# Optimization experiments

Hardware: AMD Instinct MI355X
Metric: run time of the kernel (lower is better)

The kernel has to match this reference:

```python
import jax, jax.numpy as jnp
import numpy as np
from jax import lax

H = 1024
NH = 16
R = 32
B, S = 32, 1024
LN_EPS = 1e-5

def _gelu(x):
    return jax.nn.gelu(x, approximate=False)

def setup_inputs() -> dict:
    key = jax.random.key(0)
    ks = jax.random.split(key, 24)
    w = lambda k, shape: jax.random.normal(k, shape, jnp.float32) * 0.02
    d = {}
    d['computation_results'] = jax.random.normal(ks[0], (B, S, H), jnp.float32)
    d['max_steps'] = 16
    # rule selector: Linear(H,H), GELU, Linear(H,R)
    d['rule_w1'] = w(ks[1], (H, H)); d['rule_b1'] = jnp.zeros((H,))
    d['rule_w2'] = w(ks[2], (R, H)); d['rule_b2'] = jnp.zeros((R,))
    d['rule_emb'] = jax.random.normal(ks[3], (R, H), jnp.float32)
    # MultiheadAttention packed in-proj [3H,H] and out-proj [H,H]
    d['attn_in_w'] = w(ks[4], (3 * H, H)); d['attn_in_b'] = jnp.zeros((3 * H,))
    d['attn_out_w'] = w(ks[5], (H, H)); d['attn_out_b'] = jnp.zeros((H,))
    # 2-layer LSTM, PyTorch gate order i,f,g,o
    d['lstm_wih0'] = w(ks[6], (4 * H, H)); d['lstm_whh0'] = w(ks[7], (4 * H, H))
    d['lstm_bih0'] = jnp.zeros((4 * H,)); d['lstm_bhh0'] = jnp.zeros((4 * H,))
    d['lstm_wih1'] = w(ks[8], (4 * H, H)); d['lstm_whh1'] = w(ks[9], (4 * H, H))
    d['lstm_bih1'] = jnp.zeros((4 * H,)); d['lstm_bhh1'] = jnp.zeros((4 * H,))
    # step generator: Linear(H,2H), LayerNorm(2H), GELU, Linear(2H,H)
    d['gen_w1'] = w(ks[10], (2 * H, H)); d['gen_b1'] = jnp.zeros((2 * H,))
    d['gen_ln_g'] = jnp.ones((2 * H,)); d['gen_ln_b'] = jnp.zeros((2 * H,))
    d['gen_w2'] = w(ks[11], (H, 2 * H)); d['gen_b2'] = jnp.zeros((H,))
    # step validator: Linear(2H,H), GELU, Linear(H,1), Sigmoid
    d['val_w1'] = w(ks[12], (H, 2 * H)); d['val_b1'] = jnp.zeros((H,))
    d['val_w2'] = w(ks[13], (1, H)); d['val_b2'] = jnp.zeros((1,))
    # proof verifier: Linear(H,H), GELU, Linear(H,1), Sigmoid
    d['ver_w1'] = w(ks[14], (H, H)); d['ver_b1'] = jnp.zeros((H,))
    d['ver_w2'] = w(ks[15], (1, H)); d['ver_b2'] = jnp.zeros((1,))
    return d


def reference(computation_results, max_steps, rule_w1, rule_b1, rule_w2, rule_b2, rule_emb,
              attn_in_w, attn_in_b, attn_out_w, attn_out_b,
              lstm_wih0, lstm_whh0, lstm_bih0, lstm_bhh0,
              lstm_wih1, lstm_whh1, lstm_bih1, lstm_bhh1,
              gen_w1, gen_b1, gen_ln_g, gen_ln_b, gen_w2, gen_b2,
              val_w1, val_b1, val_w2, val_b2,
              ver_w1, ver_b1, ver_w2, ver_b2):
    comp = computation_results
    b, s, h = comp.shape
    dh = h // NH
    scale = dh ** -0.5
    wq, wk, wv = jnp.split(attn_in_w, 3, axis=0)
    bq, bk, bv = jnp.split(attn_in_b, 3, axis=0)
    # K/V projections of the static context, computed once outside the step loop
    K = (comp @ wk.T + bk).reshape(b, s, NH, dh)  # [B,S,NH,dh]
    V = (comp @ wv.T + bv).reshape(b, s, NH, dh)
    lstm_params = ((lstm_wih0, lstm_whh0, lstm_bih0, lstm_bhh0),
                   (lstm_wih1, lstm_whh1, lstm_bih1, lstm_bhh1))

    def step(carry, _):
        ps, hmem, cmem = carry  # ps: [B,H]; hmem/cmem: [2,B,H]
        # rule selection
        logits = _gelu(ps @ rule_w1.T + rule_b1) @ rule_w2.T + rule_b2
        probs = jax.nn.softmax(logits, axis=-1)  # [B,R]
        sel = probs @ rule_emb  # [B,H]
        # single-query multi-head attention over computation context
        q = (ps @ wq.T + bq).reshape(b, NH, dh) * scale
        scores = jnp.einsum('bhd,bshd->bhs', q, K)
        a = jax.nn.softmax(scores, axis=-1)  # [B,NH,S]
        ctx = jnp.einsum('bhs,bshd->bhd', a, V).reshape(b, h) @ attn_out_w.T + attn_out_b
        attn_avg = a.mean(axis=1)  # head-averaged weights, [B,S]
        # 2-layer LSTM cell, one timestep
        x = ps
        hs, cs = [], []
        for l, (wih, whh, bih, bhh) in enumerate(lstm_params):
            g = x @ wih.T + bih + hmem[l] @ whh.T + bhh
            gi, gf, gg, go = jnp.split(g, 4, axis=-1)
            cn = jax.nn.sigmoid(gf) * cmem[l] + jax.nn.sigmoid(gi) * jnp.tanh(gg)
            hn = jax.nn.sigmoid(go) * jnp.tanh(cn)
            hs.append(hn); cs.append(cn); x = hn
        mem_out = x
        # step generator with LayerNorm+GELU
        si = ps + sel + ctx + mem_out
        z = si @ gen_w1.T + gen_b1
        mu = z.mean(axis=-1, keepdims=True)
        var = ((z - mu) ** 2).mean(axis=-1, keepdims=True)
        z = (z - mu) / jnp.sqrt(var + LN_EPS) * gen_ln_g + gen_ln_b
        nxt = _gelu(z) @ gen_w2.T + gen_b2
        val = jax.nn.sigmoid(_gelu(jnp.concatenate([ps, nxt], axis=-1) @ val_w1.T + val_b1) @ val_w2.T + val_b2)
        return (nxt, jnp.stack(hs), jnp.stack(cs)), (nxt, probs, val, attn_avg)

    init_state = comp[:, 0, :]
    carry0 = (init_state, jnp.zeros((2, b, h), comp.dtype), jnp.zeros((2, b, h), comp.dtype))
    (final, _, _), (steps, probs, vals, attn) = lax.scan(step, carry0, None, length=int(max_steps))
    proof_steps = jnp.concatenate([init_state[None], steps], axis=0)  # [T+1,B,H]
    proof_validity = jax.nn.sigmoid(_gelu(final @ ver_w1.T + ver_b1) @ ver_w2.T + ver_b2)  # [B,1]
    return proof_steps, proof_validity, probs, vals, attn
```

## Files before the change

### kernel.cpp

```cpp
#include <hip/hip_runtime.h>

typedef unsigned short u16;
typedef unsigned int u32;
typedef __attribute__((ext_vector_type(8))) short short8v;
typedef __attribute__((ext_vector_type(4))) float f32x4;

#define MFMA16(a,b,c) __builtin_amdgcn_mfma_f32_16x16x32_bf16((a),(b),(c),0,0,0)

__device__ __forceinline__ u16 f2bf(float f){
  u32 u = __float_as_uint(f);
  return (u16)((u + 0x7fffu + ((u >> 16) & 1u)) >> 16);
}
__device__ __forceinline__ float bf2f(u16 h){ return __uint_as_float(((u32)h) << 16); }
__device__ __forceinline__ float gelu_f(float x){ return 0.5f * x * (1.f + erff(x * 0.70710678118654752f)); }
__device__ __forceinline__ float sigm_f(float x){ return 1.f / (1.f + __expf(-x)); }
__device__ __forceinline__ void acc4(float4& a, const float4 b){ a.x+=b.x; a.y+=b.y; a.z+=b.z; a.w+=b.w; }

__device__ __forceinline__ void gl16(const void* g, void* l){
  __builtin_amdgcn_global_load_lds((const __attribute__((address_space(1))) u32*)g,
                                   (__attribute__((address_space(3))) u32*)l, 16, 0, 0);
}

struct CastJobs { const float* s[12]; u16* d[12]; int start[13]; };
__global__ __launch_bounds__(256) void cast_all_k(CastJobs J){
  int bx = blockIdx.x, j = 0;
  #pragma unroll
  for (int t = 0; t < 12; t++) if (bx >= J.start[t + 1]) j = t + 1;
  int i = (bx - J.start[j]) * 1024 + threadIdx.x * 4;
  float4 v = *(const float4*)(J.s[j] + i);
  ushort4 o; o.x = f2bf(v.x); o.y = f2bf(v.y); o.z = f2bf(v.z); o.w = f2bf(v.w);
  *(ushort4*)(J.d[j] + i) = o;
}

__global__ __launch_bounds__(256) void cast_k(const float* __restrict__ s, u16* __restrict__ d, int n){
  int i = (blockIdx.x * 256 + threadIdx.x) * 4;
  if (i + 3 < n){
    float4 v = *(const float4*)(s + i);
    ushort4 o; o.x = f2bf(v.x); o.y = f2bf(v.y); o.z = f2bf(v.z); o.w = f2bf(v.w);
    *(ushort4*)(d + i) = o;
  }
}

__global__ __launch_bounds__(256) void tcast_k(const float* __restrict__ s, u16* __restrict__ d){
  __shared__ float tile[32][33];
  int bx = blockIdx.x & 31, by = blockIdx.x >> 5;
  int tx = threadIdx.x & 31, ty = threadIdx.x >> 5;
  #pragma unroll
  for (int i = 0; i < 4; i++)
    tile[ty + i * 8][tx] = s[(size_t)(by * 32 + ty + i * 8) * 1024 + bx * 32 + tx];
  __syncthreads();
  #pragma unroll
  for (int i = 0; i < 4; i++)
    d[(size_t)(bx * 32 + ty + i * 8) * 1024 + by * 32 + tx] = f2bf(tile[tx][ty + i * 8]);
}

__global__ __launch_bounds__(256) void bias2_k(const float* __restrict__ gw1, const float* __restrict__ aob,
                                               const float* __restrict__ gb1, float* __restrict__ out){
  int j = blockIdx.x * 32 + (threadIdx.x >> 3);
  int l8 = threadIdx.x & 7;
  const float* r = gw1 + (size_t)j * 1024;
  float acc = 0.f;
  #pragma unroll 8
  for (int kk = 0; kk < 32; kk++){
    int k = kk * 32 + l8 * 4;
    float4 a = *(const float4*)(r + k);
    float4 w = *(const float4*)(aob + k);
    acc += a.x * w.x + a.y * w.y + a.z * w.z + a.w * w.w;
  }
  acc += __shfl_xor(acc, 1); acc += __shfl_xor(acc, 2); acc += __shfl_xor(acc, 4);
  if (l8 == 0) out[j] = gb1[j] + acc;
}

__global__ __launch_bounds__(256) void init_k(const float* __restrict__ comp, float* ps0, float* outp,
                                              float* h0, float* c0, float* h1, float* c1){
  int i = blockIdx.x * 256 + threadIdx.x;
  int b = i >> 10, hh = i & 1023;
  float v = comp[(size_t)b * 1048576 + hh];
  ps0[i] = v; outp[i] = v;
  h0[i] = 0.f; c0[i] = 0.f; h1[i] = 0.f; c1[i] = 0.f;
}

__global__ __launch_bounds__(256) void gemmkv_k(const u16* __restrict__ compb,
    const u16* __restrict__ Wk, const u16* __restrict__ Wv,
    const float* __restrict__ bk, const float* __restrict__ bv,
    u16* __restrict__ Kt, u16* __restrict__ Vb)
{
  __shared__ u16 Sh[16384];
  u16* As = Sh;
  u16* Bs = Sh + 8192;
  int tid = threadIdx.x;
  int x = blockIdx.x;
  int xcd = x & 7, p = x >> 3;
  int cpanel = xcd * 32 + (p >> 3);
  int wpanel = p & 7;
  int isK = (blockIdx.z != 0);
  const u16 *msrc, *nsrc; int m0, n0;
  if (!isK){ m0 = cpanel * 128; n0 = wpanel * 128; msrc = compb; nsrc = Wv; }
  else     { m0 = wpanel * 128; n0 = cpanel * 128; msrc = Wk;    nsrc = compb; }

  int w = tid >> 6, l = tid & 63, lr = l & 15, lk = l >> 4;
  int wm = (w >> 1) * 64, wn = (w & 1) * 64;
  f32x4 acc[4][4];
  #pragma unroll
  for (int i = 0; i < 4; i++)
    #pragma unroll
    for (int j = 0; j < 4; j++) acc[i][j] = (f32x4){0.f,0.f,0.f,0.f};

  for (int kc = 0; kc < 1024; kc += 64){
    #pragma unroll
    for (int r = 0; r < 4; r++){
      int s = tid + r * 256;
      int row = s >> 3, pp = s & 7;
      int lg = pp ^ (row & 7);
      gl16(msrc + (size_t)(m0 + row) * 1024 + kc + lg * 8, As + s * 8);
      gl16(nsrc + (size_t)(n0 + row) * 1024 + kc + lg * 8, Bs + s * 8);
    }
    __syncthreads();
    #pragma unroll
    for (int kk = 0; kk < 2; kk++){
      short8v a[4], bb[4];
      #pragma unroll
      for (int mi = 0; mi < 4; mi++){
        int row = wm + mi * 16 + lr;
        int ph = (kk * 4 + lk) ^ (row & 7);
        a[mi] = *(const short8v*)(As + row * 64 + ph * 8);
      }
      #pragma unroll
      for (int ni = 0; ni < 4; ni++){
        int row = wn + ni * 16 + lr;
        int ph = (kk * 4 + lk) ^ (row & 7);
        bb[ni] = *(const short8v*)(Bs + row * 64 + ph * 8);
      }
      #pragma unroll
      for (int mi = 0; mi < 4; mi++)
        #pragma unroll
        for (int ni = 0; ni < 4; ni++)
          acc[mi][ni] = MFMA16(a[mi], bb[ni], acc[mi][ni]);
    }
    __syncthreads();
  }
  #pragma unroll
  for (int mi = 0; mi < 4; mi++)
    #pragma unroll
    for (int ni = 0; ni < 4; ni++)
      #pragma unroll
      for (int r = 0; r < 4; r++){
        int row = wm + mi * 16 + lk * 4 + r;
        int col = wn + ni * 16 + lr;
        float bias = isK ? bk[m0 + row] : bv[n0 + col];
        Sh[row * 128 + col] = f2bf(acc[mi][ni][r] + bias);
      }
  __syncthreads();
  u16* dst = isK ? Kt : Vb;
  size_t base = isK ? (((size_t)(n0 >> 10) * 1024 + m0) * 1024 + (n0 & 1023))
                    : ((size_t)m0 * 1024 + n0);
  for (int i = tid; i < 2048; i += 256){
    int r = i >> 4, c8 = (i & 15) * 8;
    *(uint4*)(dst + base + (size_t)r * 1024 + c8) = *(const uint4*)(Sh + r * 128 + c8);
  }
}

__global__ __launch_bounds__(256) void gemmbb_k(const u16* __restrict__ A, const u16* __restrict__ B,
                                                u16* __restrict__ C)
{
  __shared__ u16 As[128 * 64];
  __shared__ u16 Bs[128 * 64];
  int tid = threadIdx.x;
  int m0 = blockIdx.x * 128, n0 = blockIdx.y * 128;
  int w = tid >> 6, l = tid & 63, lr = l & 15, lk = l >> 4;
  int wm = (w >> 1) * 64, wn = (w & 1) * 64;
  f32x4 acc[4][4];
  #pragma unroll
  for (int i = 0; i < 4; i++)
    #pragma unroll
    for (int j = 0; j < 4; j++) acc[i][j] = (f32x4){0.f,0.f,0.f,0.f};
  for (int kc = 0; kc < 1024; kc += 64){
    #pragma unroll
    for (int r = 0; r < 4; r++){
      int s = tid + r * 256;
      int row = s >> 3, pp = s & 7;
      int lg = pp ^ (row & 7);
      gl16(A + (size_t)(m0 + row) * 1024 + kc + lg * 8, As + s * 8);
      gl16(B + (size_t)(n0 + row) * 1024 + kc + lg * 8, Bs + s * 8);
    }
    __syncthreads();
    #pragma unroll
    for (int kk = 0; kk < 2; kk++){
      short8v a[4], bb[4];
      #pragma unroll
      for (int mi = 0; mi < 4; mi++){
        int row = wm + mi * 16 + lr;
        int ph = (kk * 4 + lk) ^ (row & 7);
        a[mi] = *(const short8v*)(As + row * 64 + ph * 8);
      }
      #pragma unroll
      for (int ni = 0; ni < 4; ni++){
        int row = wn + ni * 16 + lr;
        int ph = (kk * 4 + lk) ^ (row & 7);
        bb[ni] = *(const short8v*)(Bs + row * 64 + ph * 8);
      }
      #pragma unroll
      for (int mi = 0; mi < 4; mi++)
        #pragma unroll
        for (int ni = 0; ni < 4; ni++)
          acc[mi][ni] = MFMA16(a[mi], bb[ni], acc[mi][ni]);
    }
    __syncthreads();
  }
  #pragma unroll
  for (int mi = 0; mi < 4; mi++)
    #pragma unroll
    for (int ni = 0; ni < 4; ni++)
      #pragma unroll
      for (int r = 0; r < 4; r++){
        int row = m0 + wm + mi * 16 + lk * 4 + r;
        int col = n0 + wn + ni * 16 + lr;
        C[(size_t)row * 1024 + col] = f2bf(acc[mi][ni][r]);
      }
}

struct LinSeg {
  const float* X0; const float* Xa; const float* Xb; const float* Xc;
  const u16* W1; const float* b1;
  const float* Y; const u16* W2; const float* b2;
  float* out; float* out2;
  int K1, ld1, K2, ld2, N, act, gate;
  float scale;
  float* stats;
  const float* lng; const float* lnb; const float* lnstats;
  const float* cprev; float* cout; float* hout;
};

__device__ __forceinline__ short8v pack8(float4 v0, float4 v1){
  short8v r;
  r[0]=(short)f2bf(v0.x); r[1]=(short)f2bf(v0.y); r[2]=(short)f2bf(v0.z); r[3]=(short)f2bf(v0.w);
  r[4]=(short)f2bf(v1.x); r[5]=(short)f2bf(v1.y); r[6]=(short)f2bf(v1.z); r[7]=(short)f2bf(v1.w);
  return r;
}

__device__ __forceinline__ short8v load_sum8(const LinSeg& S, int row, int kb){
  size_t o = (size_t)row * S.K1 + kb;
  float4 v0 = *(const float4*)(S.X0 + o);
  float4 v1 = *(const float4*)(S.X0 + o + 4);
  if (S.lng){
    float mu = S.lnstats[row] * (1.f / 2048.f);
    float ms = S.lnstats[32 + row] * (1.f / 2048.f);
    float rstd = rsqrtf(ms - mu * mu + 1e-5f);
    float4 g0 = *(const float4*)(S.lng + kb), g1 = *(const float4*)(S.lng + kb + 4);
    float4 b0 = *(const float4*)(S.lnb + kb), b1 = *(const float4*)(S.lnb + kb + 4);
    v0.x = gelu_f((v0.x - mu) * rstd * g0.x + b0.x);
    v0.y = gelu_f((v0.y - mu) * rstd * g0.y + b0.y);
    v0.z = gelu_f((v0.z - mu) * rstd * g0.z + b0.z);
    v0.w = gelu_f((v0.w - mu) * rstd * g0.w + b0.w);
    v1.x = gelu_f((v1.x - mu) * rstd * g1.x + b1.x);
    v1.y = gelu_f((v1.y - mu) * rstd * g1.y + b1.y);
    v1.z = gelu_f((v1.z - mu) * rstd * g1.z + b1.z);
    v1.w = gelu_f((v1.w - mu) * rstd * g1.w + b1.w);
  } else {
    if (S.Xa){ acc4(v0, *(const float4*)(S.Xa + o)); acc4(v1, *(const float4*)(S.Xa + o + 4)); }
    if (S.Xb){ acc4(v0, *(const float4*)(S.Xb + o)); acc4(v1, *(const float4*)(S.Xb + o + 4)); }
    if (S.Xc){ acc4(v0, *(const float4*)(S.Xc + o)); acc4(v1, *(const float4*)(S.Xc + o + 4)); }
  }
  return pack8(v0, v1);
}
__device__ __forceinline__ short8v load_y8(const float* p){
  return pack8(*(const float4*)(p), *(const float4*)(p + 4));
}

typedef float Red4[32][32];

__device__ void lin_body(const LinSeg& S, int bi, int tid, Red4* red){
  int c0 = bi * 32, j0 = bi * 8;
  int w = tid >> 6, l = tid & 63, lr = l & 15, lk = l >> 4;
  int wc0 = S.gate ? ((lr >> 3) << 10) + j0 + (lr & 7) : c0 + lr;
  int wc1 = S.gate ? (((lr + 16) >> 3) << 10) + j0 + ((lr + 16) & 7) : c0 + lr + 16;
  f32x4 acc[2][2];
  #pragma unroll
  for (int i = 0; i < 2; i++)
    #pragma unroll
    for (int j = 0; j < 2; j++) acc[i][j] = (f32x4){0.f,0.f,0.f,0.f};

  {
    int chunk = S.K1 >> 2;
    int kb0 = w * chunk + lk * 8;
    for (int kk = 0; kk < chunk; kk += 32){
      int kb = kb0 + kk;
      short8v a0 = load_sum8(S, lr, kb);
      short8v a1 = load_sum8(S, lr + 16, kb);
      short8v w0 = *(const short8v*)(S.W1 + (size_t)wc0 * S.ld1 + kb);
      short8v w1 = *(const short8v*)(S.W1 + (size_t)wc1 * S.ld1 + kb);
      acc[0][0] = MFMA16(a0, w0, acc[0][0]);
      acc[0][1] = MFMA16(a0, w1, acc[0][1]);
      acc[1][0] = MFMA16(a1, w0, acc[1][0]);
      acc[1][1] = MFMA16(a1, w1, acc[1][1]);
    }
  }
  if (S.Y){
    int chunk = S.K2 >> 2;
    int kb0 = w * chunk + lk * 8;
    for (int kk = 0; kk < chunk; kk += 32){
      int kb = kb0 + kk;
      short8v a0 = load_y8(S.Y + (size_t)lr * S.K2 + kb);
      short8v a1 = load_y8(S.Y + (size_t)(lr + 16) * S.K2 + kb);
      short8v w0 = *(const short8v*)(S.W2 + (size_t)wc0 * S.ld2 + kb);
      short8v w1 = *(const short8v*)(S.W2 + (size_t)wc1 * S.ld2 + kb);
      acc[0][0] = MFMA16(a0, w0, acc[0][0]);
      acc[0][1] = MFMA16(a0, w1, acc[0][1]);
      acc[1][0] = MFMA16(a1, w0, acc[1][0]);
      acc[1][1] = MFMA16(a1, w1, acc[1][1]);
    }
  }
  #pragma unroll
  for (int mi = 0; mi < 2; mi++)
    #pragma unroll
    for (int ni = 0; ni < 2; ni++)
      #pragma unroll
      for (int r = 0; r < 4; r++)
        red[w][mi * 16 + lk * 4 + r][ni * 16 + lr] = acc[mi][ni][r];
  __syncthreads();
  if (S.gate){
    int row = tid >> 3, j = tid & 7;
    float s[4];
    #pragma unroll
    for (int g = 0; g < 4; g++){
      float v = 0.f;
      #pragma unroll
      for (int ww = 0; ww < 4; ww++) v += red[ww][row][g * 8 + j];
      s[g] = v;
    }
    int gc = j0 + j;
    float gI = s[0] + S.b1[gc]        + S.b2[gc];
    float gF = s[1] + S.b1[1024 + gc] + S.b2[1024 + gc];
    float gG = s[2] + S.b1[2048 + gc] + S.b2[2048 + gc];
    float gO = s[3] + S.b1[3072 + gc] + S.b2[3072 + gc];
    int idx = row * 1024 + gc;
    float cN = sigm_f(gF) * S.cprev[idx] + sigm_f(gI) * tanhf(gG);
    S.cout[idx] = cN;
    S.hout[idx] = sigm_f(gO) * tanhf(cN);
    return;
  }
  float vout[4]; int iout[4];
  int cnt = 0;
  for (int i = tid; i < 1024; i += 256){
    int row = i >> 5, col = i & 31;
    float v = 0.f;
    #pragma unroll
    for (int ww = 0; ww < 4; ww++) v += red[ww][row][col];
    v += S.b1[c0 + col];
    if (S.b2) v += S.b2[c0 + col];
    if (S.act == 1) v = gelu_f(v);
    else if (S.act == 2) v *= S.scale;
    S.out[(size_t)row * S.N + c0 + col] = v;
    if (S.out2) S.out2[(size_t)row * S.N + c0 + col] = v;
    vout[cnt] = v; iout[cnt] = i; cnt++;
  }
  if (S.stats){
    __syncthreads();
    float* rf = (float*)red;
    #pragma unroll
    for (int q2 = 0; q2 < 4; q2++){
      rf[iout[q2]] = vout[q2];
      rf[1024 + iout[q2]] = vout[q2] * vout[q2];
    }
    __syncthreads();
    if (tid < 32){
      float s = 0.f, s2 = 0.f;
      #pragma unroll
      for (int cc = 0; cc < 32; cc++){ s += rf[tid * 32 + cc]; s2 += rf[1024 + tid * 32 + cc]; }
      atomicAdd(S.stats + tid, s);
      atomicAdd(S.stats + 32 + tid, s2);
    }
  }
}

__global__ __launch_bounds__(256) void linmulti_k(LinSeg s0, LinSeg s1, LinSeg s2, int n0, int n1){
  __shared__ float red[4][32][32];
  int bx = blockIdx.x, tid = threadIdx.x;
  if (bx < n0) lin_body(s0, bx, tid, red);
  else if (bx < n0 + n1) lin_body(s1, bx - n0, tid, red);
  else lin_body(s2, bx - n0 - n1, tid, red);
}

__device__ void attn_job(int bh, int tid, const float* q, const u16* Kt, const u16* Vb,
                         float* afull, float* ctx0, float* shf){
  float* qs = shf;
  float* sc = shf + 64;
  float* rmx = shf + 1088;
  float* rsm = shf + 1092;
  float* ctxp = shf + 1096;
  int b = bh >> 4, h = bh & 15;
  if (tid < 64) qs[tid] = q[bh * 64 + tid];
  __syncthreads();
  const u32* kt = (const u32*)(Kt + (size_t)bh * 65536);
  float a0 = 0.f, a1 = 0.f, a2 = 0.f, a3 = 0.f;
  #pragma unroll 8
  for (int d = 0; d < 64; d++){
    float qd = qs[d];
    u32 p0 = kt[d * 512 + tid];
    u32 p1 = kt[d * 512 + tid + 256];
    a0 += qd * bf2f((u16)(p0 & 0xffff)); a1 += qd * bf2f((u16)(p0 >> 16));
    a2 += qd * bf2f((u16)(p1 & 0xffff)); a3 += qd * bf2f((u16)(p1 >> 16));
  }
  float mx = fmaxf(fmaxf(a0, a1), fmaxf(a2, a3));
  for (int o = 1; o < 64; o <<= 1) mx = fmaxf(mx, __shfl_xor(mx, o));
  if ((tid & 63) == 0) rmx[tid >> 6] = mx;
  __syncthreads();
  mx = fmaxf(fmaxf(rmx[0], rmx[1]), fmaxf(rmx[2], rmx[3]));
  float e0 = __expf(a0 - mx), e1 = __expf(a1 - mx), e2 = __expf(a2 - mx), e3 = __expf(a3 - mx);
  float sm = e0 + e1 + e2 + e3;
  for (int o = 1; o < 64; o <<= 1) sm += __shfl_xor(sm, o);
  if ((tid & 63) == 0) rsm[tid >> 6] = sm;
  __syncthreads();
  sm = rsm[0] + rsm[1] + rsm[2] + rsm[3];
  float inv = 1.f / sm;
  float* ar = afull + (size_t)bh * 1024;
  float2 w0 = make_float2(e0 * inv, e1 * inv);
  float2 w1 = make_float2(e2 * inv, e3 * inv);
  *(float2*)(sc + 2 * tid) = w0;       *(float2*)(ar + 2 * tid) = w0;
  *(float2*)(sc + 512 + 2 * tid) = w1; *(float2*)(ar + 512 + 2 * tid) = w1;
  __syncthreads();
  int d2 = (tid & 31) * 2, chunk = tid >> 5;
  const u16* vb = Vb + ((size_t)(b * 1024) * 16 + h) * 64 + d2;
  float c0 = 0.f, c1 = 0.f;
  for (int s = chunk * 128; s < chunk * 128 + 128; s++){
    u32 vv = *(const u32*)(vb + (size_t)s * 1024);
    float wv = sc[s];
    c0 += wv * bf2f((u16)(vv & 0xffff));
    c1 += wv * bf2f((u16)(vv >> 16));
  }
  *(float2*)(ctxp + chunk * 64 + d2) = make_float2(c0, c1);
  __syncthreads();
  if (tid < 64){
    float r = 0.f;
    #pragma unroll
    for (int c = 0; c < 8; c++) r += ctxp[c * 64 + tid];
    ctx0[bh * 64 + tid] = r;
  }
}

__device__ void rule2_job(int b, int tid, const float* h1a, const float* w2, const float* b2,
                          const float* emb, float* probs_out, float* sel, float* shf){
  float* lg = shf;
  float* psh = shf + 32;
  int j = tid >> 3, l8 = tid & 7;
  const float* xr = h1a + b * 1024;
  const float* wr = w2 + j * 1024;
  float acc = 0.f;
  #pragma unroll 8
  for (int kk = 0; kk < 32; kk++){
    int k = kk * 32 + l8 * 4;
    float4 xv = *(const float4*)(xr + k);
    float4 wv = *(const float4*)(wr + k);
    acc += xv.x * wv.x + xv.y * wv.y + xv.z * wv.z + xv.w * wv.w;
  }
  acc += __shfl_xor(acc, 1); acc += __shfl_xor(acc, 2); acc += __shfl_xor(acc, 4);
  if (l8 == 0) lg[j] = acc + b2[j];
  __syncthreads();
  if (tid < 32){
    float v = lg[tid];
    float m = v;
    for (int o = 1; o < 32; o <<= 1) m = fmaxf(m, __shfl_xor(m, o));
    float e = __expf(v - m);
    float s = e;
    for (int o = 1; o < 32; o <<= 1) s += __shfl_xor(s, o);
    float p = e / s;
    psh[tid] = p;
    probs_out[b * 32 + tid] = p;
  }
  __syncthreads();
  for (int j2 = tid; j2 < 1024; j2 += 256){
    float a2 = 0.f;
    #pragma unroll
    for (int r = 0; r < 32; r++) a2 += psh[r] * emb[r * 1024 + j2];
    sel[b * 1024 + j2] = a2;
  }
}

struct D2Params {
  const float* qbuf;
  const u16* Kt; const u16* Vb; float* afull; float* ctx0;
  const float* h1a; const float* w2; const float* b2r; const float* emb;
  float* probs_out; float* sel;
  LinSeg sL1; float* lnstats;
};
__global__ __launch_bounds__(256) void step_d2_k(D2Params P){
  __shared__ float red[4][32][32];
  float* shf = &red[0][0][0];
  int bx = blockIdx.x, tid = threadIdx.x;
  if (bx < 512){ attn_job(bx, tid, P.qbuf, P.Kt, P.Vb, P.afull, P.ctx0, shf); return; }
  if (bx < 544){ rule2_job(bx - 512, tid, P.h1a, P.w2, P.b2r, P.emb, P.probs_out, P.sel, shf); return; }
  if (bx < 672){ lin_body(P.sL1, bx - 544, tid, red); return; }
  if (tid < 64) P.lnstats[tid] = 0.f;
}

__global__ __launch_bounds__(256) void valver_k(const u16* __restrict__ vw1, const float* __restrict__ vb1,
    const u16* __restrict__ verw1, const float* __restrict__ verb1,
    const float* __restrict__ proof, float* __restrict__ v1){
  __shared__ float red[4][32][32];
  int t = blockIdx.y;
  LinSeg S = {};
  if (t < 16){
    S.X0 = proof + (size_t)t * 32768; S.K1 = 1024; S.W1 = vw1; S.ld1 = 2048; S.b1 = vb1;
    S.Y = proof + (size_t)(t + 1) * 32768; S.K2 = 1024; S.W2 = vw1 + 1024; S.ld2 = 2048;
  } else {
    S.X0 = proof + (size_t)16 * 32768; S.K1 = 1024; S.W1 = verw1; S.ld1 = 1024; S.b1 = verb1;
  }
  S.out = v1 + (size_t)t * 32768; S.N = 1024; S.act = 1;
  lin_body(S, blockIdx.x, threadIdx.x, red);
}

__global__ __launch_bounds__(256) void dotsig_b_k(const float* __restrict__ v1,
    const float* __restrict__ w2v, const float* __restrict__ b2v,
    const float* __restrict__ w2ver, const float* __restrict__ b2ver,
    float* __restrict__ out_vals, float* __restrict__ out_valid){
  int t = blockIdx.x;
  const float* w = (t < 16) ? w2v : w2ver;
  const float* bs = (t < 16) ? b2v : b2ver;
  const float* x = v1 + (size_t)t * 32768;
  int b = threadIdx.x >> 3, l8 = threadIdx.x & 7;
  const float* xr = x + (size_t)b * 1024;
  float acc = 0.f;
  #pragma unroll 8
  for (int kk = 0; kk < 32; kk++){
    int k = kk * 32 + l8 * 4;
    float4 xv = *(const float4*)(xr + k);
    float4 wv = *(const float4*)(w + k);
    acc += xv.x * wv.x + xv.y * wv.y + xv.z * wv.z + xv.w * wv.w;
  }
  acc += __shfl_xor(acc, 1); acc += __shfl_xor(acc, 2); acc += __shfl_xor(acc, 4);
  if (l8 == 0){
    float r = sigm_f(acc + bs[0]);
    if (t < 16) out_vals[t * 32 + b] = r; else out_valid[b] = r;
  }
}

__global__ __launch_bounds__(256) void attnavg_all_k(const float* __restrict__ afull, float* __restrict__ out){
  int idx = blockIdx.x * 256 + threadIdx.x;
  int t = idx >> 15, r = idx & 32767;
  int b = r >> 10, s = r & 1023;
  const float* base = afull + (size_t)t * 524288 + (size_t)b * 16384;
  float acc = 0.f;
  #pragma unroll
  for (int h = 0; h < 16; h++) acc += base[h * 1024 + s];
  out[idx] = acc * (1.f / 16.f);
}

extern "C" void kernel_launch(void* const* d_in, const int* in_sizes, int n_in,
                              void* d_out, int out_size, void* d_ws, size_t ws_size,
                              hipStream_t stream) {
  const float* comp      = (const float*)d_in[0];
  const float* rule_w1   = (const float*)d_in[2];
  const float* rule_b1   = (const float*)d_in[3];
  const float* rule_w2   = (const float*)d_in[4];
  const float* rule_b2   = (const float*)d_in[5];
  const float* rule_emb  = (const float*)d_in[6];
  const float* attn_in_w = (const float*)d_in[7];
  const float* attn_in_b = (const float*)d_in[8];
  const float* attn_out_w= (const float*)d_in[9];
  const float* attn_out_b= (const float*)d_in[10];
  const float* wih0 = (const float*)d_in[11];
  const float* whh0 = (const float*)d_in[12];
  const float* bih0 = (const float*)d_in[13];
  const float* bhh0 = (const float*)d_in[14];
  const float* wih1 = (const float*)d_in[15];
  const float* whh1 = (const float*)d_in[16];
  const float* bih1 = (const float*)d_in[17];
  const float* bhh1 = (const float*)d_in[18];
  const float* gen_w1 = (const float*)d_in[19];
  const float* gen_b1 = (const float*)d_in[20];
  const float* ln_g   = (const float*)d_in[21];
  const float* ln_b   = (const float*)d_in[22];
  const float* gen_w2 = (const float*)d_in[23];
  const float* gen_b2 = (const float*)d_in[24];
  const float* val_w1 = (const float*)d_in[25];
  const float* val_b1 = (const float*)d_in[26];
  const float* val_w2 = (const float*)d_in[27];
  const float* val_b2 = (const float*)d_in[28];
  const float* ver_w1 = (const float*)d_in[29];
  const float* ver_b1 = (const float*)d_in[30];
  const float* ver_w2 = (const float*)d_in[31];
  const float* ver_b2 = (const float*)d_in[32];

  float* out_f     = (float*)d_out;
  float* out_proof = out_f;
  float* out_valid = out_f + 17 * 32768;
  float* out_probs = out_valid + 32;
  float* out_vals  = out_probs + 16 * 1024;
  float* out_attn  = out_vals + 16 * 32;

  char* wp = (char*)d_ws;
  auto carve = [&](size_t bytes) -> void* {
    void* p = (void*)wp; wp += (bytes + 255) & ~(size_t)255; return p;
  };
  u16* Kt    = (u16*)carve((size_t)33554432 * 2);
  u16* Vb    = (u16*)carve((size_t)33554432 * 2);
  u16* compb = (u16*)carve((size_t)33554432 * 2);
  float* afull_all = (float*)compb;
  u16* rw1b  = (u16*)carve(2097152);
  u16* wqb   = (u16*)carve(2097152);
  u16* wkb   = (u16*)carve(2097152);
  u16* wvb   = (u16*)carve(2097152);
  u16* aowTb = (u16*)carve(2097152);
  u16* wih0b = (u16*)carve(8388608);
  u16* whh0b = (u16*)carve(8388608);
  u16* wih1b = (u16*)carve(8388608);
  u16* whh1b = (u16*)carve(8388608);
  u16* gw1b  = (u16*)carve(4194304);
  u16* gw2b  = (u16*)carve(4194304);
  u16* vw1b  = (u16*)carve(4194304);
  u16* verw1b= (u16*)carve(2097152);
  u16* gaw   = (u16*)carve(4194304);
  float* bias2 = (float*)carve(8192);
  float* psb[2]  = { (float*)carve(131072), (float*)carve(131072) };
  float* h0b[2]  = { (float*)carve(131072), (float*)carve(131072) };
  float* c0b[2]  = { (float*)carve(131072), (float*)carve(131072) };
  float* h1b[2]  = { (float*)carve(131072), (float*)carve(131072) };
  float* c1b[2]  = { (float*)carve(131072), (float*)carve(131072) };
  float* h1act = (float*)carve(131072);
  float* sel   = (float*)carve(131072);
  float* qbuf  = (float*)carve(131072);
  float* ctx0  = (float*)carve(131072);
  float* zbuf  = (float*)carve(262144);
  float* v1buf = (float*)carve(2228224);
  float* lnstats = (float*)carve(256);
  (void)ws_size; (void)in_sizes; (void)n_in; (void)out_size;

  CastJobs J;
  const float* srcs[12] = { rule_w1, attn_in_w, attn_in_w + 1048576, attn_in_w + 2097152,
                            wih0, whh0, wih1, whh1, gen_w1, gen_w2, val_w1, ver_w1 };
  u16* dsts[12] = { rw1b, wqb, wkb, wvb, wih0b, whh0b, wih1b, whh1b, gw1b, gw2b, vw1b, verw1b };
  int sizes[12] = { 1048576, 1048576, 1048576, 1048576,
                    4194304, 4194304, 4194304, 4194304, 2097152, 2097152, 2097152, 1048576 };
  int st = 0;
  for (int i = 0; i < 12; i++){ J.s[i] = srcs[i]; J.d[i] = dsts[i]; J.start[i] = st; st += sizes[i] / 1024; }
  J.start[12] = st;
  cast_all_k<<<dim3(st), dim3(256), 0, stream>>>(J);
  tcast_k<<<dim3(1024), dim3(256), 0, stream>>>(attn_out_w, aowTb);
  cast_k<<<dim3(32768), dim3(256), 0, stream>>>(comp, compb, 33554432);

  gemmkv_k<<<dim3(2048, 1, 2), dim3(256), 0, stream>>>(compb, wkb, wvb,
      attn_in_b + 1024, attn_in_b + 2048, Kt, Vb);
  gemmbb_k<<<dim3(16, 8), dim3(256), 0, stream>>>(gw1b, aowTb, gaw);
  bias2_k<<<dim3(64), dim3(256), 0, stream>>>(gen_w1, attn_out_b, gen_b1, bias2);

  init_k<<<dim3(128), dim3(256), 0, stream>>>(comp, psb[0], out_proof,
      h0b[0], c0b[0], h1b[0], c1b[0]);

  for (int t = 0; t < 16; t++){
    int cur = t & 1, nx = cur ^ 1;
    float* ps = psb[cur];
    float* afull_t = afull_all + (size_t)t * 524288;
    LinSeg sRule = {}; sRule.X0 = ps; sRule.K1 = 1024; sRule.W1 = rw1b; sRule.ld1 = 1024;
    sRule.b1 = rule_b1; sRule.out = h1act; sRule.N = 1024; sRule.act = 1;
    LinSeg sQ = {}; sQ.X0 = ps; sQ.K1 = 1024; sQ.W1 = wqb; sQ.ld1 = 1024; sQ.b1 = attn_in_b;
    sQ.out = qbuf; sQ.N = 1024; sQ.act = 2; sQ.scale = 0.125f;
    LinSeg sL0 = {}; sL0.X0 = ps; sL0.K1 = 1024; sL0.W1 = wih0b; sL0.ld1 = 1024; sL0.b1 = bih0;
    sL0.Y = h0b[cur]; sL0.K2 = 1024; sL0.W2 = whh0b; sL0.ld2 = 1024; sL0.b2 = bhh0;
    sL0.gate = 1; sL0.cprev = c0b[cur]; sL0.cout = c0b[nx]; sL0.hout = h0b[nx];
    linmulti_k<<<dim3(192), dim3(256), 0, stream>>>(sRule, sQ, sL0, 32, 32);
    D2Params P;
    P.qbuf = qbuf;
    P.Kt = Kt; P.Vb = Vb; P.afull = afull_t; P.ctx0 = ctx0;
    P.h1a = h1act; P.w2 = rule_w2; P.b2r = rule_b2; P.emb = rule_emb;
    P.probs_out = out_probs + t * 1024; P.sel = sel;
    LinSeg sL1 = {}; sL1.X0 = h0b[nx]; sL1.K1 = 1024; sL1.W1 = wih1b; sL1.ld1 = 1024; sL1.b1 = bih1;
    sL1.Y = h1b[cur]; sL1.K2 = 1024; sL1.W2 = whh1b; sL1.ld2 = 1024; sL1.b2 = bhh1;
    sL1.gate = 1; sL1.cprev = c1b[cur]; sL1.cout = c1b[nx]; sL1.hout = h1b[nx];
    P.sL1 = sL1; P.lnstats = lnstats;
    step_d2_k<<<dim3(673), dim3(256), 0, stream>>>(P);
    LinSeg sG1 = {}; sG1.X0 = ps; sG1.Xa = sel; sG1.Xb = h1b[nx];
    sG1.K1 = 1024; sG1.W1 = gw1b; sG1.ld1 = 1024; sG1.b1 = bias2;
    sG1.Y = ctx0; sG1.K2 = 1024; sG1.W2 = gaw; sG1.ld2 = 1024;
    sG1.out = zbuf; sG1.N = 2048; sG1.stats = lnstats;
    linmulti_k<<<dim3(64), dim3(256), 0, stream>>>(sG1, sG1, sG1, 64, 0);
    LinSeg sG2 = {}; sG2.X0 = zbuf; sG2.K1 = 2048; sG2.W1 = gw2b; sG2.ld1 = 2048; sG2.b1 = gen_b2;
    sG2.out = psb[nx]; sG2.N = 1024; sG2.out2 = out_proof + (size_t)(t + 1) * 32768;
    sG2.lng = ln_g; sG2.lnb = ln_b; sG2.lnstats = lnstats;
    linmulti_k<<<dim3(32), dim3(256), 0, stream>>>(sG2, sG2, sG2, 32, 0);
  }
  valver_k<<<dim3(32, 17), dim3(256), 0, stream>>>(vw1b, val_b1, verw1b, ver_b1, out_proof, v1buf);
  dotsig_b_k<<<dim3(17), dim3(256), 0, stream>>>(v1buf, val_w2, val_b2, ver_w2, ver_b2,
      out_vals, out_valid);
  attnavg_all_k<<<dim3(2048), dim3(256), 0, stream>>>(afull_all, out_attn);
}
```

Baseline: 2.105 ms.

## Halve per-block tile width, split gen2 along K, and relayout V per head

```diff
diff --git a/kernel.cpp b/kernel.cpp
--- a/kernel.cpp
+++ b/kernel.cpp
@@ -21,24 +21,15 @@
                                    (__attribute__((address_space(3))) u32*)l, 16, 0, 0);
 }
 
-struct CastJobs { const float* s[12]; u16* d[12]; int start[13]; };
+struct CastJobs { const float* s[13]; u16* d[13]; int start[14]; };
 __global__ __launch_bounds__(256) void cast_all_k(CastJobs J){
   int bx = blockIdx.x, j = 0;
   #pragma unroll
-  for (int t = 0; t < 12; t++) if (bx >= J.start[t + 1]) j = t + 1;
+  for (int t = 0; t < 13; t++) if (bx >= J.start[t + 1]) j = t + 1;
   int i = (bx - J.start[j]) * 1024 + threadIdx.x * 4;
   float4 v = *(const float4*)(J.s[j] + i);
   ushort4 o; o.x = f2bf(v.x); o.y = f2bf(v.y); o.z = f2bf(v.z); o.w = f2bf(v.w);
   *(ushort4*)(J.d[j] + i) = o;
-}
-
-__global__ __launch_bounds__(256) void cast_k(const float* __restrict__ s, u16* __restrict__ d, int n){
-  int i = (blockIdx.x * 256 + threadIdx.x) * 4;
-  if (i + 3 < n){
-    float4 v = *(const float4*)(s + i);
-    ushort4 o; o.x = f2bf(v.x); o.y = f2bf(v.y); o.z = f2bf(v.z); o.w = f2bf(v.w);
-    *(ushort4*)(d + i) = o;
-  }
 }
 
 __global__ __launch_bounds__(256) void tcast_k(const float* __restrict__ s, u16* __restrict__ d){
@@ -71,12 +62,12 @@
   if (l8 == 0) out[j] = gb1[j] + acc;
 }
 
-__global__ __launch_bounds__(256) void init_k(const float* __restrict__ comp, float* ps0, float* outp,
-                                              float* h0, float* c0, float* h1, float* c1){
+__global__ __launch_bounds__(256) void init_k(const float* __restrict__ comp, float* psa, float* psbz,
+                                              float* outp, float* h0, float* c0, float* h1, float* c1){
   int i = blockIdx.x * 256 + threadIdx.x;
   int b = i >> 10, hh = i & 1023;
   float v = comp[(size_t)b * 1048576 + hh];
-  ps0[i] = v; outp[i] = v;
+  psa[i] = v; psbz[i] = 0.f; outp[i] = v;
   h0[i] = 0.f; c0[i] = 0.f; h1[i] = 0.f; c1[i] = 0.f;
 }
 
@@ -151,12 +142,19 @@
         Sh[row * 128 + col] = f2bf(acc[mi][ni][r] + bias);
       }
   __syncthreads();
-  u16* dst = isK ? Kt : Vb;
-  size_t base = isK ? (((size_t)(n0 >> 10) * 1024 + m0) * 1024 + (n0 & 1023))
-                    : ((size_t)m0 * 1024 + n0);
   for (int i = tid; i < 2048; i += 256){
     int r = i >> 4, c8 = (i & 15) * 8;
-    *(uint4*)(dst + base + (size_t)r * 1024 + c8) = *(const uint4*)(Sh + r * 128 + c8);
+    uint4 o = *(const uint4*)(Sh + r * 128 + c8);
+    if (!isK){
+      int bs = m0 + r, hd = n0 + c8;
+      int b = bs >> 10, s = bs & 1023;
+      int h = hd >> 6, d = hd & 63;
+      *(uint4*)(Vb + ((size_t)(b * 16 + h) * 1024 + s) * 64 + d) = o;
+    } else {
+      int hd = m0 + r, bs = n0 + c8;
+      int b = bs >> 10, s = bs & 1023;
+      *(uint4*)(Kt + ((size_t)b * 1024 + hd) * 1024 + s) = o;
+    }
   }
 }
 
@@ -224,7 +222,7 @@
   const u16* W1; const float* b1;
   const float* Y; const u16* W2; const float* b2;
   float* out; float* out2;
-  int K1, ld1, K2, ld2, N, act, gate;
+  int K1, ldx, ld1, K2, ld2, N, act, gate;
   float scale;
   float* stats;
   const float* lng; const float* lnb; const float* lnstats;
@@ -239,7 +237,7 @@
 }
 
 __device__ __forceinline__ short8v load_sum8(const LinSeg& S, int row, int kb){
-  size_t o = (size_t)row * S.K1 + kb;
+  size_t o = (size_t)row * S.ldx + kb;
   float4 v0 = *(const float4*)(S.X0 + o);
   float4 v1 = *(const float4*)(S.X0 + o + 4);
   if (S.lng){
@@ -267,18 +265,15 @@
   return pack8(*(const float4*)(p), *(const float4*)(p + 4));
 }
 
-typedef float Red4[32][32];
-
-__device__ void lin_body(const LinSeg& S, int bi, int tid, Red4* red){
-  int c0 = bi * 32, j0 = bi * 8;
+typedef float Red16[32][16];
+
+__device__ void lin_body(const LinSeg& S, int bi, int tid, Red16* red){
+  int c0 = bi * 16, j0 = bi * 4;
   int w = tid >> 6, l = tid & 63, lr = l & 15, lk = l >> 4;
-  int wc0 = S.gate ? ((lr >> 3) << 10) + j0 + (lr & 7) : c0 + lr;
-  int wc1 = S.gate ? (((lr + 16) >> 3) << 10) + j0 + ((lr + 16) & 7) : c0 + lr + 16;
-  f32x4 acc[2][2];
-  #pragma unroll
-  for (int i = 0; i < 2; i++)
-    #pragma unroll
-    for (int j = 0; j < 2; j++) acc[i][j] = (f32x4){0.f,0.f,0.f,0.f};
+  int wc0 = S.gate ? ((lr >> 2) << 10) + j0 + (lr & 3) : c0 + lr;
+  f32x4 acc[2];
+  acc[0] = (f32x4){0.f,0.f,0.f,0.f};
+  acc[1] = (f32x4){0.f,0.f,0.f,0.f};
 
   {
     int chunk = S.K1 >> 2;
@@ -288,11 +283,8 @@
       short8v a0 = load_sum8(S, lr, kb);
       short8v a1 = load_sum8(S, lr + 16, kb);
       short8v w0 = *(const short8v*)(S.W1 + (size_t)wc0 * S.ld1 + kb);
-      short8v w1 = *(const short8v*)(S.W1 + (size_t)wc1 * S.ld1 + kb);
-      acc[0][0] = MFMA16(a0, w0, acc[0][0]);
-      acc[0][1] = MFMA16(a0, w1, acc[0][1]);
-      acc[1][0] = MFMA16(a1, w0, acc[1][0]);
-      acc[1][1] = MFMA16(a1, w1, acc[1][1]);
+      acc[0] = MFMA16(a0, w0, acc[0]);
+      acc[1] = MFMA16(a1, w0, acc[1]);
     }
   }
   if (S.Y){
@@ -303,50 +295,47 @@
       short8v a0 = load_y8(S.Y + (size_t)lr * S.K2 + kb);
       short8v a1 = load_y8(S.Y + (size_t)(lr + 16) * S.K2 + kb);
       short8v w0 = *(const short8v*)(S.W2 + (size_t)wc0 * S.ld2 + kb);
-      short8v w1 = *(const short8v*)(S.W2 + (size_t)wc1 * S.ld2 + kb);
-      acc[0][0] = MFMA16(a0, w0, acc[0][0]);
-      acc[0][1] = MFMA16(a0, w1, acc[0][1]);
-      acc[1][0] = MFMA16(a1, w0, acc[1][0]);
-      acc[1][1] = MFMA16(a1, w1, acc[1][1]);
+      acc[0] = MFMA16(a0, w0, acc[0]);
+      acc[1] = MFMA16(a1, w0, acc[1]);
     }
   }
   #pragma unroll
   for (int mi = 0; mi < 2; mi++)
     #pragma unroll
-    for (int ni = 0; ni < 2; ni++)
-      #pragma unroll
-      for (int r = 0; r < 4; r++)
-        red[w][mi * 16 + lk * 4 + r][ni * 16 + lr] = acc[mi][ni][r];
+    for (int r = 0; r < 4; r++)
+      red[w][mi * 16 + lk * 4 + r][lr] = acc[mi][r];
   __syncthreads();
   if (S.gate){
-    int row = tid >> 3, j = tid & 7;
-    float s[4];
-    #pragma unroll
-    for (int g = 0; g < 4; g++){
-      float v = 0.f;
-      #pragma unroll
-      for (int ww = 0; ww < 4; ww++) v += red[ww][row][g * 8 + j];
-      s[g] = v;
-    }
-    int gc = j0 + j;
-    float gI = s[0] + S.b1[gc]        + S.b2[gc];
-    float gF = s[1] + S.b1[1024 + gc] + S.b2[1024 + gc];
-    float gG = s[2] + S.b1[2048 + gc] + S.b2[2048 + gc];
-    float gO = s[3] + S.b1[3072 + gc] + S.b2[3072 + gc];
-    int idx = row * 1024 + gc;
-    float cN = sigm_f(gF) * S.cprev[idx] + sigm_f(gI) * tanhf(gG);
-    S.cout[idx] = cN;
-    S.hout[idx] = sigm_f(gO) * tanhf(cN);
+    if (tid < 128){
+      int row = tid >> 2, j = tid & 3;
+      float s[4];
+      #pragma unroll
+      for (int g = 0; g < 4; g++){
+        float v = 0.f;
+        #pragma unroll
+        for (int ww = 0; ww < 4; ww++) v += red[ww][row][g * 4 + j];
+        s[g] = v;
+      }
+      int gc = j0 + j;
+      float gI = s[0] + S.b1[gc]        + S.b2[gc];
+      float gF = s[1] + S.b1[1024 + gc] + S.b2[1024 + gc];
+      float gG = s[2] + S.b1[2048 + gc] + S.b2[2048 + gc];
+      float gO = s[3] + S.b1[3072 + gc] + S.b2[3072 + gc];
+      int idx = row * 1024 + gc;
+      float cN = sigm_f(gF) * S.cprev[idx] + sigm_f(gI) * tanhf(gG);
+      S.cout[idx] = cN;
+      S.hout[idx] = sigm_f(gO) * tanhf(cN);
+    }
     return;
   }
-  float vout[4]; int iout[4];
+  float vout[2]; int iout[2];
   int cnt = 0;
-  for (int i = tid; i < 1024; i += 256){
-    int row = i >> 5, col = i & 31;
+  for (int i = tid; i < 512; i += 256){
+    int row = i >> 4, col = i & 15;
     float v = 0.f;
     #pragma unroll
     for (int ww = 0; ww < 4; ww++) v += red[ww][row][col];
-    v += S.b1[c0 + col];
+    if (S.b1) v += S.b1[c0 + col];
     if (S.b2) v += S.b2[c0 + col];
     if (S.act == 1) v = gelu_f(v);
     else if (S.act == 2) v *= S.scale;
@@ -357,16 +346,13 @@
   if (S.stats){
     __syncthreads();
     float* rf = (float*)red;
-    #pragma unroll
-    for (int q2 = 0; q2 < 4; q2++){
-      rf[iout[q2]] = vout[q2];
-      rf[1024 + iout[q2]] = vout[q2] * vout[q2];
-    }
+    rf[iout[0]] = vout[0]; rf[512 + iout[0]] = vout[0] * vout[0];
+    rf[iout[1]] = vout[1]; rf[512 + iout[1]] = vout[1] * vout[1];
     __syncthreads();
     if (tid < 32){
       float s = 0.f, s2 = 0.f;
       #pragma unroll
-      for (int cc = 0; cc < 32; cc++){ s += rf[tid * 32 + cc]; s2 += rf[1024 + tid * 32 + cc]; }
+      for (int cc = 0; cc < 16; cc++){ s += rf[tid * 16 + cc]; s2 += rf[512 + tid * 16 + cc]; }
       atomicAdd(S.stats + tid, s);
       atomicAdd(S.stats + 32 + tid, s2);
     }
@@ -374,7 +360,7 @@
 }
 
 __global__ __launch_bounds__(256) void linmulti_k(LinSeg s0, LinSeg s1, LinSeg s2, int n0, int n1){
-  __shared__ float red[4][32][32];
+  __shared__ float red[4][32][16];
   int bx = blockIdx.x, tid = threadIdx.x;
   if (bx < n0) lin_body(s0, bx, tid, red);
   else if (bx < n0 + n1) lin_body(s1, bx - n0, tid, red);
@@ -385,8 +371,7 @@
                          float* afull, float* ctx0, float* shf){
   float* qs = shf;
   float* sc = shf + 64;
-  float* rmx = shf + 1088;
-  float* rsm = shf + 1092;
+  float* rr = shf + 1088;
   float* ctxp = shf + 1096;
   int b = bh >> 4, h = bh & 15;
   if (tid < 64) qs[tid] = q[bh * 64 + tid];
@@ -403,15 +388,15 @@
   }
   float mx = fmaxf(fmaxf(a0, a1), fmaxf(a2, a3));
   for (int o = 1; o < 64; o <<= 1) mx = fmaxf(mx, __shfl_xor(mx, o));
-  if ((tid & 63) == 0) rmx[tid >> 6] = mx;
-  __syncthreads();
-  mx = fmaxf(fmaxf(rmx[0], rmx[1]), fmaxf(rmx[2], rmx[3]));
+  if ((tid & 63) == 0) rr[tid >> 6] = mx;
+  __syncthreads();
+  mx = fmaxf(fmaxf(rr[0], rr[1]), fmaxf(rr[2], rr[3]));
   float e0 = __expf(a0 - mx), e1 = __expf(a1 - mx), e2 = __expf(a2 - mx), e3 = __expf(a3 - mx);
   float sm = e0 + e1 + e2 + e3;
   for (int o = 1; o < 64; o <<= 1) sm += __shfl_xor(sm, o);
-  if ((tid & 63) == 0) rsm[tid >> 6] = sm;
-  __syncthreads();
-  sm = rsm[0] + rsm[1] + rsm[2] + rsm[3];
+  if ((tid & 63) == 0) rr[4 + (tid >> 6)] = sm;
+  __syncthreads();
+  sm = rr[4] + rr[5] + rr[6] + rr[7];
   float inv = 1.f / sm;
   float* ar = afull + (size_t)bh * 1024;
   float2 w0 = make_float2(e0 * inv, e1 * inv);
@@ -419,16 +404,18 @@
   *(float2*)(sc + 2 * tid) = w0;       *(float2*)(ar + 2 * tid) = w0;
   *(float2*)(sc + 512 + 2 * tid) = w1; *(float2*)(ar + 512 + 2 * tid) = w1;
   __syncthreads();
-  int d2 = (tid & 31) * 2, chunk = tid >> 5;
-  const u16* vb = Vb + ((size_t)(b * 1024) * 16 + h) * 64 + d2;
+  int dd2 = tid & 31, chunk = tid >> 5;
+  const u32* vp = (const u32*)(Vb + ((size_t)(b * 16 + h) * 1024 + chunk * 128) * 64) + dd2;
+  const float* scp = sc + chunk * 128;
   float c0 = 0.f, c1 = 0.f;
-  for (int s = chunk * 128; s < chunk * 128 + 128; s++){
-    u32 vv = *(const u32*)(vb + (size_t)s * 1024);
-    float wv = sc[s];
-    c0 += wv * bf2f((u16)(vv & 0xffff));
-    c1 += wv * bf2f((u16)(vv >> 16));
-  }
-  *(float2*)(ctxp + chunk * 64 + d2) = make_float2(c0, c1);
+  #pragma unroll 8
+  for (int s = 0; s < 128; s++){
+    u32 vv = vp[s * 32];
+    float w = scp[s];
+    c0 += w * bf2f((u16)(vv & 0xffff));
+    c1 += w * bf2f((u16)(vv >> 16));
+  }
+  *(float2*)(ctxp + chunk * 64 + dd2 * 2) = make_float2(c0, c1);
   __syncthreads();
   if (tid < 64){
     float r = 0.f;
@@ -476,6 +463,20 @@
   }
 }
 
+__global__ __launch_bounds__(256) void step_d1_k(LinSeg sRule, LinSeg sQ, LinSeg sL0,
+                                                 const float* pa, const float* pb, float* proof_t){
+  __shared__ float red[4][32][16];
+  int bx = blockIdx.x, tid = threadIdx.x;
+  if (bx < 64){ lin_body(sRule, bx, tid, red); return; }
+  if (bx < 128){ lin_body(sQ, bx - 64, tid, red); return; }
+  if (bx < 384){ lin_body(sL0, bx - 128, tid, red); return; }
+  int i = (bx - 384) * 1024 + tid * 4;
+  float4 va = *(const float4*)(pa + i);
+  float4 vb = *(const float4*)(pb + i);
+  acc4(va, vb);
+  *(float4*)(proof_t + i) = va;
+}
+
 struct D2Params {
   const float* qbuf;
   const u16* Kt; const u16* Vb; float* afull; float* ctx0;
@@ -484,26 +485,36 @@
   LinSeg sL1; float* lnstats;
 };
 __global__ __launch_bounds__(256) void step_d2_k(D2Params P){
-  __shared__ float red[4][32][32];
+  __shared__ float red[4][32][16];
   float* shf = &red[0][0][0];
   int bx = blockIdx.x, tid = threadIdx.x;
   if (bx < 512){ attn_job(bx, tid, P.qbuf, P.Kt, P.Vb, P.afull, P.ctx0, shf); return; }
   if (bx < 544){ rule2_job(bx - 512, tid, P.h1a, P.w2, P.b2r, P.emb, P.probs_out, P.sel, shf); return; }
-  if (bx < 672){ lin_body(P.sL1, bx - 544, tid, red); return; }
+  if (bx < 800){ lin_body(P.sL1, bx - 544, tid, red); return; }
   if (tid < 64) P.lnstats[tid] = 0.f;
+}
+
+__global__ __launch_bounds__(256) void fixup_k(const float* __restrict__ pa, const float* __restrict__ pb,
+                                               float* __restrict__ out){
+  int i = blockIdx.x * 1024 + threadIdx.x * 4;
+  float4 va = *(const float4*)(pa + i);
+  float4 vb = *(const float4*)(pb + i);
+  acc4(va, vb);
+  *(float4*)(out + i) = va;
 }
 
 __global__ __launch_bounds__(256) void valver_k(const u16* __restrict__ vw1, const float* __restrict__ vb1,
     const u16* __restrict__ verw1, const float* __restrict__ verb1,
-    const float* __restrict__ proof, float* __restrict__ v1){
-  __shared__ float red[4][32][32];
+    const float* __restrict__ proof, const float* __restrict__ pfa, const float* __restrict__ pfb,
+    float* __restrict__ v1){
+  __shared__ float red[4][32][16];
   int t = blockIdx.y;
   LinSeg S = {};
   if (t < 16){
-    S.X0 = proof + (size_t)t * 32768; S.K1 = 1024; S.W1 = vw1; S.ld1 = 2048; S.b1 = vb1;
+    S.X0 = proof + (size_t)t * 32768; S.K1 = 1024; S.ldx = 1024; S.W1 = vw1; S.ld1 = 2048; S.b1 = vb1;
     S.Y = proof + (size_t)(t + 1) * 32768; S.K2 = 1024; S.W2 = vw1 + 1024; S.ld2 = 2048;
   } else {
-    S.X0 = proof + (size_t)16 * 32768; S.K1 = 1024; S.W1 = verw1; S.ld1 = 1024; S.b1 = verb1;
+    S.X0 = pfa; S.Xa = pfb; S.K1 = 1024; S.ldx = 1024; S.W1 = verw1; S.ld1 = 1024; S.b1 = verb1;
   }
   S.out = v1 + (size_t)t * 32768; S.N = 1024; S.act = 1;
   lin_body(S, blockIdx.x, threadIdx.x, red);
@@ -611,11 +622,12 @@
   u16* verw1b= (u16*)carve(2097152);
   u16* gaw   = (u16*)carve(4194304);
   float* bias2 = (float*)carve(8192);
-  float* psb[2]  = { (float*)carve(131072), (float*)carve(131072) };
-  float* h0b[2]  = { (float*)carve(131072), (float*)carve(131072) };
-  float* c0b[2]  = { (float*)carve(131072), (float*)carve(131072) };
-  float* h1b[2]  = { (float*)carve(131072), (float*)carve(131072) };
-  float* c1b[2]  = { (float*)carve(131072), (float*)carve(131072) };
+  float* psa[2] = { (float*)carve(131072), (float*)carve(131072) };
+  float* psq[2] = { (float*)carve(131072), (float*)carve(131072) };
+  float* h0b[2] = { (float*)carve(131072), (float*)carve(131072) };
+  float* c0b[2] = { (float*)carve(131072), (float*)carve(131072) };
+  float* h1b[2] = { (float*)carve(131072), (float*)carve(131072) };
+  float* c1b[2] = { (float*)carve(131072), (float*)carve(131072) };
   float* h1act = (float*)carve(131072);
   float* sel   = (float*)carve(131072);
   float* qbuf  = (float*)carve(131072);
@@ -626,59 +638,68 @@
   (void)ws_size; (void)in_sizes; (void)n_in; (void)out_size;
 
   CastJobs J;
-  const float* srcs[12] = { rule_w1, attn_in_w, attn_in_w + 1048576, attn_in_w + 2097152,
-                            wih0, whh0, wih1, whh1, gen_w1, gen_w2, val_w1, ver_w1 };
-  u16* dsts[12] = { rw1b, wqb, wkb, wvb, wih0b, whh0b, wih1b, whh1b, gw1b, gw2b, vw1b, verw1b };
-  int sizes[12] = { 1048576, 1048576, 1048576, 1048576,
-                    4194304, 4194304, 4194304, 4194304, 2097152, 2097152, 2097152, 1048576 };
+  const float* srcs[13] = { rule_w1, attn_in_w, attn_in_w + 1048576, attn_in_w + 2097152,
+                            wih0, whh0, wih1, whh1, gen_w1, gen_w2, val_w1, ver_w1, comp };
+  u16* dsts[13] = { rw1b, wqb, wkb, wvb, wih0b, whh0b, wih1b, whh1b, gw1b, gw2b, vw1b, verw1b, compb };
+  int sizes[13] = { 1048576, 1048576, 1048576, 1048576,
+                    4194304, 4194304, 4194304, 4194304, 2097152, 2097152, 2097152, 1048576, 33554432 };
   int st = 0;
-  for (int i = 0; i < 12; i++){ J.s[i] = srcs[i]; J.d[i] = dsts[i]; J.start[i] = st; st += sizes[i] / 1024; }
-  J.start[12] = st;
+  for (int i = 0; i < 13; i++){ J.s[i] = srcs[i]; J.d[i] = dsts[i]; J.start[i] = st; st += sizes[i] / 1024; }
+  J.start[13] = st;
   cast_all_k<<<dim3(st), dim3(256), 0, stream>>>(J);
   tcast_k<<<dim3(1024), dim3(256), 0, stream>>>(attn_out_w, aowTb);
-  cast_k<<<dim3(32768), dim3(256), 0, stream>>>(comp, compb, 33554432);
 
   gemmkv_k<<<dim3(2048, 1, 2), dim3(256), 0, stream>>>(compb, wkb, wvb,
       attn_in_b + 1024, attn_in_b + 2048, Kt, Vb);
   gemmbb_k<<<dim3(16, 8), dim3(256), 0, stream>>>(gw1b, aowTb, gaw);
   bias2_k<<<dim3(64), dim3(256), 0, stream>>>(gen_w1, attn_out_b, gen_b1, bias2);
 
-  init_k<<<dim3(128), dim3(256), 0, stream>>>(comp, psb[0], out_proof,
+  init_k<<<dim3(128), dim3(256), 0, stream>>>(comp, psa[0], psq[0], out_proof,
       h0b[0], c0b[0], h1b[0], c1b[0]);
 
   for (int t = 0; t < 16; t++){
     int cur = t & 1, nx = cur ^ 1;
-    float* ps = psb[cur];
+    float* pa = psa[cur];
+    float* pb = psq[cur];
     float* afull_t = afull_all + (size_t)t * 524288;
-    LinSeg sRule = {}; sRule.X0 = ps; sRule.K1 = 1024; sRule.W1 = rw1b; sRule.ld1 = 1024;
-    sRule.b1 = rule_b1; sRule.out = h1act; sRule.N = 1024; sRule.act = 1;
-    LinSeg sQ = {}; sQ.X0 = ps; sQ.K1 = 1024; sQ.W1 = wqb; sQ.ld1 = 1024; sQ.b1 = attn_in_b;
-    sQ.out = qbuf; sQ.N = 1024; sQ.act = 2; sQ.scale = 0.125f;
-    LinSeg sL0 = {}; sL0.X0 = ps; sL0.K1 = 1024; sL0.W1 = wih0b; sL0.ld1 = 1024; sL0.b1 = bih0;
+    LinSeg sRule = {}; sRule.X0 = pa; sRule.Xa = pb; sRule.K1 = 1024; sRule.ldx = 1024;
+    sRule.W1 = rw1b; sRule.ld1 = 1024; sRule.b1 = rule_b1; sRule.out = h1act; sRule.N = 1024; sRule.act = 1;
+    LinSeg sQ = {}; sQ.X0 = pa; sQ.Xa = pb; sQ.K1 = 1024; sQ.ldx = 1024;
+    sQ.W1 = wqb; sQ.ld1 = 1024; sQ.b1 = attn_in_b; sQ.out = qbuf; sQ.N = 1024; sQ.act = 2; sQ.scale = 0.125f;
+    LinSeg sL0 = {}; sL0.X0 = pa; sL0.Xa = pb; sL0.K1 = 1024; sL0.ldx = 1024;
+    sL0.W1 = wih0b; sL0.ld1 = 1024; sL0.b1 = bih0;
     sL0.Y = h0b[cur]; sL0.K2 = 1024; sL0.W2 = whh0b; sL0.ld2 = 1024; sL0.b2 = bhh0;
     sL0.gate = 1; sL0.cprev = c0b[cur]; sL0.cout = c0b[nx]; sL0.hout = h0b[nx];
-    linmulti_k<<<dim3(192), dim3(256), 0, stream>>>(sRule, sQ, sL0, 32, 32);
+    step_d1_k<<<dim3(416), dim3(256), 0, stream>>>(sRule, sQ, sL0, pa, pb,
+        out_proof + (size_t)t * 32768);
     D2Params P;
-    P.qbuf = qbuf;
-    P.Kt = Kt; P.Vb = Vb; P.afull = afull_t; P.ctx0 = ctx0;
+    P.qbuf = qbuf; P.Kt = Kt; P.Vb = Vb; P.afull = afull_t; P.ctx0 = ctx0;
     P.h1a = h1act; P.w2 = rule_w2; P.b2r = rule_b2; P.emb = rule_emb;
     P.probs_out = out_probs + t * 1024; P.sel = sel;
-    LinSeg sL1 = {}; sL1.X0 = h0b[nx]; sL1.K1 = 1024; sL1.W1 = wih1b; sL1.ld1 = 1024; sL1.b1 = bih1;
+    LinSeg sL1 = {}; sL1.X0 = h0b[nx]; sL1.K1 = 1024; sL1.ldx = 1024;
+    sL1.W1 = wih1b; sL1.ld1 = 1024; sL1.b1 = bih1;
     sL1.Y = h1b[cur]; sL1.K2 = 1024; sL1.W2 = whh1b; sL1.ld2 = 1024; sL1.b2 = bhh1;
     sL1.gate = 1; sL1.cprev = c1b[cur]; sL1.cout = c1b[nx]; sL1.hout = h1b[nx];
     P.sL1 = sL1; P.lnstats = lnstats;
-    step_d2_k<<<dim3(673), dim3(256), 0, stream>>>(P);
-    LinSeg sG1 = {}; sG1.X0 = ps; sG1.Xa = sel; sG1.Xb = h1b[nx];
-    sG1.K1 = 1024; sG1.W1 = gw1b; sG1.ld1 = 1024; sG1.b1 = bias2;
+    step_d2_k<<<dim3(801), dim3(256), 0, stream>>>(P);
+    LinSeg sG1 = {}; sG1.X0 = pa; sG1.Xa = pb; sG1.Xb = sel; sG1.Xc = h1b[nx];
+    sG1.K1 = 1024; sG1.ldx = 1024; sG1.W1 = gw1b; sG1.ld1 = 1024; sG1.b1 = bias2;
     sG1.Y = ctx0; sG1.K2 = 1024; sG1.W2 = gaw; sG1.ld2 = 1024;
     sG1.out = zbuf; sG1.N = 2048; sG1.stats = lnstats;
-    linmulti_k<<<dim3(64), dim3(256), 0, stream>>>(sG1, sG1, sG1, 64, 0);
-    LinSeg sG2 = {}; sG2.X0 = zbuf; sG2.K1 = 2048; sG2.W1 = gw2b; sG2.ld1 = 2048; sG2.b1 = gen_b2;
-    sG2.out = psb[nx]; sG2.N = 1024; sG2.out2 = out_proof + (size_t)(t + 1) * 32768;
-    sG2.lng = ln_g; sG2.lnb = ln_b; sG2.lnstats = lnstats;
-    linmulti_k<<<dim3(32), dim3(256), 0, stream>>>(sG2, sG2, sG2, 32, 0);
-  }
-  valver_k<<<dim3(32, 17), dim3(256), 0, stream>>>(vw1b, val_b1, verw1b, ver_b1, out_proof, v1buf);
+    linmulti_k<<<dim3(128), dim3(256), 0, stream>>>(sG1, sG1, sG1, 128, 0);
+    LinSeg sA = {}; sA.X0 = zbuf; sA.K1 = 1024; sA.ldx = 2048;
+    sA.W1 = gw2b; sA.ld1 = 2048; sA.b1 = gen_b2;
+    sA.lng = ln_g; sA.lnb = ln_b; sA.lnstats = lnstats;
+    sA.out = psa[nx]; sA.N = 1024;
+    LinSeg sB = {}; sB.X0 = zbuf + 1024; sB.K1 = 1024; sB.ldx = 2048;
+    sB.W1 = gw2b + 1024; sB.ld1 = 2048;
+    sB.lng = ln_g + 1024; sB.lnb = ln_b + 1024; sB.lnstats = lnstats;
+    sB.out = psq[nx]; sB.N = 1024;
+    linmulti_k<<<dim3(128), dim3(256), 0, stream>>>(sA, sB, sB, 64, 64);
+  }
+  fixup_k<<<dim3(32), dim3(256), 0, stream>>>(psa[0], psq[0], out_proof + (size_t)16 * 32768);
+  valver_k<<<dim3(64, 17), dim3(256), 0, stream>>>(vw1b, val_b1, verw1b, ver_b1,
+      out_proof, psa[0], psq[0], v1buf);
   dotsig_b_k<<<dim3(17), dim3(256), 0, stream>>>(v1buf, val_w2, val_b2, ver_w2, ver_b2,
       out_vals, out_valid);
   attnavg_all_k<<<dim3(2048), dim3(256), 0, stream>>>(afull_all, out_attn);
```

New measurement: 2.019 ms. 1.04x faster.
